# Optimization experiments

Hardware: AMD Instinct MI355X
Metric: run time of the kernel (lower is better)

Reference implementation:

```python
import jax, jax.numpy as jnp
import numpy as np
import math

B, S, HID = 128, 200, 1024
NH = 4
DK = HID // NH
LSESS = 200  # session_len
MAXSEQ = 200
EPS = 1e-12


def setup_inputs() -> dict:
    key = jax.random.key(0)
    ks = jax.random.split(key, 12)
    inp = {}
    inp['query'] = jax.random.normal(ks[0], (B, S, HID), jnp.float32)
    inp['key'] = jax.random.normal(ks[1], (B, S, HID), jnp.float32)
    inp['value'] = jax.random.normal(ks[2], (B, S, HID), jnp.float32)
    std = 0.05
    inp['attn_w0'] = std * jax.random.normal(ks[3], (DK, DK), jnp.float32)
    inp['attn_w1'] = std * jax.random.normal(ks[4], (DK, DK), jnp.float32)
    inp['attn_w2'] = std * jax.random.normal(ks[5], (DK, DK), jnp.float32)
    inp['attn_w3'] = std * jax.random.normal(ks[6], (LSESS, DK), jnp.float32)
    inp['attn_bias'] = jnp.zeros((DK,), jnp.float32)
    inp['complex_weight'] = 0.02 * jax.random.normal(ks[7], (1, NH, MAXSEQ // 2 + 1, DK, 2), jnp.float32)
    bound = 1.0 / math.sqrt(HID)
    inp['linear_w'] = jax.random.uniform(ks[8], (HID, HID), jnp.float32, -bound, bound)
    inp['linear_b'] = jax.random.uniform(ks[9], (HID,), jnp.float32, -bound, bound)
    inp['ln_w'] = jnp.ones((HID,), jnp.float32)
    inp['ln_b'] = jnp.zeros((HID,), jnp.float32)
    return inp


def _gelu(x):
    return x * 0.5 * (1.0 + jax.lax.erf(x / jnp.sqrt(jnp.asarray(2.0, x.dtype))))


def reference(query, key, value, attn_w0, attn_w1, attn_w2, attn_w3, attn_bias,
              complex_weight, linear_w, linear_b, ln_w, ln_b):
    nb = query.shape[0]
    # (B, S, H, DK) -> (B, H, S, DK)
    def split_heads(x):
        return x.reshape(nb, -1, NH, DK).transpose(0, 2, 1, 3)
    q, k, v = split_heads(query), split_heads(key), split_heads(value)

    q = q @ attn_w0
    k = k @ attn_w1
    v = v @ attn_w2

    qf = jnp.fft.rfft(q, axis=2, norm='ortho')   # (B,H,S//2+1,DK) complex
    kf = jnp.fft.rfft(k, axis=2, norm='ortho')
    weight = complex_weight[..., 0] + 1j * complex_weight[..., 1]  # (1,4,MAXSEQ//2+1,DK)
    res = qf * jnp.conj(kf) * weight
    corr = jnp.fft.irfft(res, n=MAXSEQ, axis=2, norm='ortho')       # (B,H,MAXSEQ,DK)

    alpha = jnp.matmul(jax.nn.relu(corr + attn_bias), attn_w3.T)    # (B,H,MAXSEQ,LSESS)
    alpha = jax.nn.softmax(alpha, axis=-2)                          # softmax over seq dim
    x = jnp.einsum('bhsl,bhsd->bhld', alpha, v)                     # (B,H,LSESS,DK)

    x = x.transpose(0, 2, 1, 3).reshape(nb, -1, NH * DK)            # (B,LSESS,HID)
    x = x @ linear_w.T + linear_b
    # dropout is identity at inference
    x = _gelu(x)
    # LayerNorm (TF-style, eps inside sqrt)
    u = x.mean(-1, keepdims=True)
    s = ((x - u) ** 2).mean(-1, keepdims=True)
    x = (x - u) / jnp.sqrt(s + EPS)
    return ln_w * x + ln_b
```

## Files before the change

### kernel.cpp

```cpp
#include <hip/hip_runtime.h>
#include <hip/hip_bf16.h>
#include <math.h>

#define BATCH 128
#define SEQ   200
#define HID   1024
#define NH    4
#define DK    256
#define NF    101
#define NF2   202
#define LS    200
#define PD    256

typedef __attribute__((ext_vector_type(8))) short bf16x8;
typedef __attribute__((ext_vector_type(4))) float f32x4;

__device__ __forceinline__ unsigned short f2bf(float f) {
    union { float f; unsigned u; } v; v.f = f;
    unsigned r = v.u + 0x7fff + ((v.u >> 16) & 1);
    return (unsigned short)(r >> 16);
}
__device__ __forceinline__ float bf2f(unsigned short h) {
    union { unsigned u; float f; } v; v.u = ((unsigned)h) << 16;
    return v.f;
}

__device__ __forceinline__ void gld_lds16(const void* g, void* l) {
    __builtin_amdgcn_global_load_lds(
        (const __attribute__((address_space(1))) unsigned*)g,
        (__attribute__((address_space(3))) unsigned*)l, 16, 0, 0);
}

#define KSWZ(row, c8) ((c8) ^ (((row) & 7) << 3))

__global__ void init_tables_bf16(unsigned short* __restrict__ F, unsigned short* __restrict__ G) {
    int idx = blockIdx.x * 256 + threadIdx.x;
    const double inv = 0.07071067811865475244;
    const double PI2 = 6.283185307179586476925;
    {
        int fidx = idx >> 8, s = idx & 255;
        double v = 0.0;
        if (s < SEQ && fidx < NF2) {
            int f = (fidx < NF) ? fidx : fidx - NF;
            double ang = PI2 * (double)((f * s) % SEQ) / (double)SEQ;
            v = (fidx < NF) ? cos(ang) * inv : -sin(ang) * inv;
        }
        F[idx] = f2bf((float)v);
    }
    {
        int s = idx >> 8, j = idx & 255;
        double v = 0.0;
        if (s < SEQ && j < NF2) {
            if (j < NF) {
                double al = (j == 0 || j == NF - 1) ? 1.0 : 2.0;
                v = al * cos(PI2 * (double)((j * s) % SEQ) / (double)SEQ) * inv;
            } else {
                int f = j - NF;
                if (f != 0 && f != NF - 1)
                    v = -2.0 * sin(PI2 * (double)((f * s) % SEQ) / (double)SEQ) * inv;
            }
        }
        G[idx] = f2bf((float)v);
    }
}

__global__ void wtrans256(const float* __restrict__ src, unsigned short* __restrict__ dst) {
    int dout = blockIdx.x, din = threadIdx.x;
    dst[dout * 256 + din] = f2bf(src[din * 256 + dout]);
}

__global__ void w3pad(const float* __restrict__ src, unsigned short* __restrict__ dst) {
    int row = blockIdx.x, col = threadIdx.x;
    dst[row * 256 + col] = (row < LS) ? f2bf(src[row * 256 + col]) : (unsigned short)0;
}

__global__ void fconv(const float* __restrict__ src, unsigned short* __restrict__ dst, int n) {
    int i = blockIdx.x * 256 + threadIdx.x;
    if (i < n) dst[i] = f2bf(src[i]);
}

__global__ __launch_bounds__(256)
void mgemm128(const unsigned short* __restrict__ A, const float* __restrict__ Bf0,
              unsigned short* __restrict__ C0,
              int K, int lda, int ldb, int ldc,
              long aOuter, long aInner, long bOuter, long bInner,
              long cOuter, long cInner, int nInner, int nbValid) {
    int bz = blockIdx.z;
    int bo = bz / nInner, bi = bz - bo * nInner;
    const unsigned short* Ab = A + bo * aOuter + bi * aInner;
    const float* Bf = Bf0 + bo * bOuter + bi * bInner;

    __shared__ unsigned short As[128 * 64];
    __shared__ unsigned short Bs[128 * 64];

    int t = threadIdx.x;
    int m0 = blockIdx.y * 128, n0 = blockIdx.x * 128;
    int lane = t & 63, wave = t >> 6;
    int wr = wave >> 1, wc = wave & 1;
    int la = lane & 15, hi = lane >> 4;

    f32x4 acc[4][4] = {};
    int rsub = t >> 3;
    int c8 = (t & 7) * 8;

    for (int k0 = 0; k0 < K; k0 += 64) {
#pragma unroll
        for (int p = 0; p < 4; ++p) {
            int row = p * 32 + rsub;
            gld_lds16(Ab + (long)(m0 + row) * lda + k0 + KSWZ(row, c8), &As[row * 64 + c8]);
        }
#pragma unroll
        for (int p = 0; p < 4; ++p) {
            int row = p * 32 + rsub;
            int gn = n0 + row;
            unsigned short tmp[8];
            if (gn < nbValid) {
                const float4* src = reinterpret_cast<const float4*>(Bf + (long)gn * ldb + k0 + c8);
                float4 x0 = src[0], x1 = src[1];
                tmp[0] = f2bf(x0.x); tmp[1] = f2bf(x0.y); tmp[2] = f2bf(x0.z); tmp[3] = f2bf(x0.w);
                tmp[4] = f2bf(x1.x); tmp[5] = f2bf(x1.y); tmp[6] = f2bf(x1.z); tmp[7] = f2bf(x1.w);
            } else {
#pragma unroll
                for (int j = 0; j < 8; ++j) tmp[j] = 0;
            }
            *(bf16x8*)&Bs[row * 64 + KSWZ(row, c8)] = *(bf16x8*)tmp;
        }
        __syncthreads();
#pragma unroll
        for (int half = 0; half < 2; ++half) {
            int ko = half * 32 + hi * 8;
            bf16x8 a[4], b[4];
#pragma unroll
            for (int mi = 0; mi < 4; ++mi) {
                int ra = wr * 64 + mi * 16 + la;
                a[mi] = *(const bf16x8*)&As[ra * 64 + KSWZ(ra, ko)];
            }
#pragma unroll
            for (int ni = 0; ni < 4; ++ni) {
                int rb = wc * 64 + ni * 16 + la;
                b[ni] = *(const bf16x8*)&Bs[rb * 64 + KSWZ(rb, ko)];
            }
#pragma unroll
            for (int mi = 0; mi < 4; ++mi)
#pragma unroll
                for (int ni = 0; ni < 4; ++ni)
                    acc[mi][ni] = __builtin_amdgcn_mfma_f32_16x16x32_bf16(a[mi], b[ni], acc[mi][ni], 0, 0, 0);
        }
        __syncthreads();
    }

    unsigned short* Ch = C0 + bo * cOuter + bi * cInner;
#pragma unroll
    for (int mi = 0; mi < 4; ++mi) {
#pragma unroll
        for (int ni = 0; ni < 4; ++ni) {
            int gn = n0 + wc * 64 + ni * 16 + la;
            int gmB = m0 + wr * 64 + mi * 16 + hi * 4;
#pragma unroll
            for (int rr = 0; rr < 4; ++rr)
                Ch[(long)(gmB + rr) * ldc + gn] = f2bf(acc[mi][ni][rr]);
        }
    }
}

template <int EPI, bool XCDSWZ>
__global__ __launch_bounds__(512, 2)
void mgemm256(const unsigned short* __restrict__ A, const unsigned short* __restrict__ B,
              unsigned short* __restrict__ C0, int K, int lda, int ldb, int ldc,
              long aOuter, long aInner, long bOuter, long bInner,
              long cOuter, long cInner, int nInner, int mValid,
              const float* __restrict__ biasN) {
    extern __shared__ unsigned short lds[];
    unsigned short* AsB = lds;
    unsigned short* BsB = lds + 32768;

    int bx = blockIdx.x, by = blockIdx.y;
    if (XCDSWZ) {
        int nwg = gridDim.x * gridDim.y;
        int flat = by * gridDim.x + bx;
        int cpx = nwg >> 3;
        int swz = (flat & 7) * cpx + (flat >> 3);
        bx = swz % gridDim.x; by = swz / gridDim.x;
    }
    int bz = blockIdx.z;
    int bo = bz / nInner, bi = bz - bo * nInner;
    const unsigned short* Ab = A + bo * aOuter + bi * aInner;
    const unsigned short* Bb = B + bo * bOuter + bi * bInner;

    int t = threadIdx.x;
    int m0 = by * 256, n0 = bx * 256;
    int lane = t & 63, wave = t >> 6;
    int wr = wave >> 2, wc = wave & 3;
    int la = lane & 15, hi = lane >> 4;

    f32x4 acc[8][4] = {};
    int rsub = t >> 3;
    int c8 = (t & 7) * 8;

    auto STAGE = [&](int buf, int kt) {
        int k0 = kt << 6;
        unsigned short* Asb = AsB + buf * 16384;
        unsigned short* Bsb = BsB + buf * 16384;
#pragma unroll
        for (int p = 0; p < 4; ++p) {
            int row = p * 64 + rsub;
            int ksw = k0 + KSWZ(row, c8);
            gld_lds16(Ab + (long)(m0 + row) * lda + ksw, &Asb[row * 64 + c8]);
            gld_lds16(Bb + (long)(n0 + row) * ldb + ksw, &Bsb[row * 64 + c8]);
        }
    };

    int nkt = K >> 6;
    STAGE(0, 0);

    for (int kt = 0; kt < nkt; ++kt) {
        int cur = kt & 1;
        if (kt + 1 < nkt) {
            STAGE(cur ^ 1, kt + 1);
            asm volatile("s_waitcnt vmcnt(8)" ::: "memory");
        } else {
            asm volatile("s_waitcnt vmcnt(0)" ::: "memory");
        }
        __builtin_amdgcn_s_barrier();
        const unsigned short* Acur = AsB + cur * 16384;
        const unsigned short* Bcur = BsB + cur * 16384;
#pragma unroll
        for (int half = 0; half < 2; ++half) {
            int ko = half * 32 + hi * 8;
            bf16x8 a[8], b[4];
#pragma unroll
            for (int mi = 0; mi < 8; ++mi) {
                int ra = wr * 128 + mi * 16 + la;
                a[mi] = *(const bf16x8*)&Acur[ra * 64 + KSWZ(ra, ko)];
            }
#pragma unroll
            for (int ni = 0; ni < 4; ++ni) {
                int rb = wc * 64 + ni * 16 + la;
                b[ni] = *(const bf16x8*)&Bcur[rb * 64 + KSWZ(rb, ko)];
            }
            __builtin_amdgcn_s_setprio(1);
#pragma unroll
            for (int mi = 0; mi < 8; ++mi)
#pragma unroll
                for (int ni = 0; ni < 4; ++ni)
                    acc[mi][ni] = __builtin_amdgcn_mfma_f32_16x16x32_bf16(a[mi], b[ni], acc[mi][ni], 0, 0, 0);
            __builtin_amdgcn_s_setprio(0);
        }
        __builtin_amdgcn_s_barrier();
    }

    unsigned short* Ch = C0 + bo * cOuter + bi * cInner;
#pragma unroll
    for (int mi = 0; mi < 8; ++mi) {
#pragma unroll
        for (int ni = 0; ni < 4; ++ni) {
            int gn = n0 + wc * 64 + ni * 16 + la;
            int gmB = m0 + wr * 128 + mi * 16 + hi * 4;
            float bN = 0.f;
            if (EPI == 2 || EPI == 4) bN = biasN[gn];
#pragma unroll
            for (int rr = 0; rr < 4; ++rr) {
                int gm = gmB + rr;
                if (gm >= mValid) continue;
                float v = acc[mi][ni][rr];
                if (EPI == 0) Ch[(long)gm * ldc + gn] = f2bf(v);
                else if (EPI == 2) Ch[(long)gm * ldc + gn] = f2bf(fmaxf(v + bN, 0.f));
                else Ch[(long)gm * ldc + gn] = f2bf(v + bN);
            }
        }
    }
}

__global__ void crossspec(unsigned short* __restrict__ QF, const unsigned short* __restrict__ KF,
                          const float* __restrict__ cw) {
    long idx = (long)blockIdx.x * 256 + threadIdx.x;
    if (idx >= (long)BATCH * NH * DK * NF) return;
    int f = (int)(idx % NF);
    long tq = idx / NF;
    int d = (int)(tq % DK);
    int bh = (int)(tq / DK);
    int h = bh & (NH - 1);
    long base = (long)bh * DK * PD + (long)d * PD;
    float qr = bf2f(QF[base + f]), qi = bf2f(QF[base + NF + f]);
    float kr = bf2f(KF[base + f]), ki = bf2f(KF[base + NF + f]);
    float cr = qr * kr + qi * ki;
    float ci = qi * kr - qr * ki;
    long wb = (((long)h * NF + f) * DK + d) * 2;
    float wr = cw[wb], wi = cw[wb + 1];
    QF[base + f]      = f2bf(cr * wr - ci * wi);
    QF[base + NF + f] = f2bf(cr * wi + ci * wr);
    if (f < PD - NF2) QF[base + NF2 + f] = 0;
}

__global__ __launch_bounds__(256) void softmax_rows(const unsigned short* __restrict__ in,
                                                    unsigned short* __restrict__ out) {
    long row = (long)blockIdx.x * 4 + (threadIdx.x >> 6);
    int lane = threadIdx.x & 63;
    const unsigned short* p = in + row * PD;
    float v[4];
    float m = -1e30f;
#pragma unroll
    for (int i = 0; i < 4; ++i) {
        int s = lane + 64 * i;
        v[i] = (s < SEQ) ? bf2f(p[s]) : -1e30f;
        m = fmaxf(m, v[i]);
    }
#pragma unroll
    for (int o = 32; o; o >>= 1) m = fmaxf(m, __shfl_xor(m, o));
    float e[4], sum = 0.f;
#pragma unroll
    for (int i = 0; i < 4; ++i) {
        int s = lane + 64 * i;
        e[i] = (s < SEQ) ? expf(v[i] - m) : 0.f;
        sum += e[i];
    }
#pragma unroll
    for (int o = 32; o; o >>= 1) sum += __shfl_xor(sum, o);
    float inv = 1.f / sum;
    unsigned short* q = out + row * PD;
#pragma unroll
    for (int i = 0; i < 4; ++i) {
        int s = lane + 64 * i;
        q[s] = (s < SEQ) ? f2bf(e[i] * inv) : (unsigned short)0;
    }
}

__global__ __launch_bounds__(256) void gelu_ln_kernel(const unsigned short* __restrict__ y2,
                               const float* __restrict__ lnw, const float* __restrict__ lnb,
                               float* __restrict__ out) {
    long row = blockIdx.x;
    int tid = threadIdx.x;
    const short4* xr = reinterpret_cast<const short4*>(y2 + row * HID);
    short4 h4 = xr[tid];
    float g[4];
    {
        float x0 = bf2f((unsigned short)h4.x), x1 = bf2f((unsigned short)h4.y);
        float x2 = bf2f((unsigned short)h4.z), x3 = bf2f((unsigned short)h4.w);
        g[0] = 0.5f * x0 * (1.f + erff(x0 * 0.70710678118654752f));
        g[1] = 0.5f * x1 * (1.f + erff(x1 * 0.70710678118654752f));
        g[2] = 0.5f * x2 * (1.f + erff(x2 * 0.70710678118654752f));
        g[3] = 0.5f * x3 * (1.f + erff(x3 * 0.70710678118654752f));
    }

    __shared__ float red[4];
    float s = g[0] + g[1] + g[2] + g[3];
#pragma unroll
    for (int o = 32; o > 0; o >>= 1) s += __shfl_down(s, o);
    if ((tid & 63) == 0) red[tid >> 6] = s;
    __syncthreads();
    float mean = (red[0] + red[1] + red[2] + red[3]) * (1.f / (float)HID);

    float v2 = 0.f;
#pragma unroll
    for (int p = 0; p < 4; ++p) { float d = g[p] - mean; v2 += d * d; }
    __syncthreads();
#pragma unroll
    for (int o = 32; o > 0; o >>= 1) v2 += __shfl_down(v2, o);
    if ((tid & 63) == 0) red[tid >> 6] = v2;
    __syncthreads();
    float var = (red[0] + red[1] + red[2] + red[3]) * (1.f / (float)HID);
    float rstd = rsqrtf(var + 1e-12f);

    float4 o4;
    int i0 = tid * 4;
    o4.x = (g[0] - mean) * rstd * lnw[i0 + 0] + lnb[i0 + 0];
    o4.y = (g[1] - mean) * rstd * lnw[i0 + 1] + lnb[i0 + 1];
    o4.z = (g[2] - mean) * rstd * lnw[i0 + 2] + lnb[i0 + 2];
    o4.w = (g[3] - mean) * rstd * lnw[i0 + 3] + lnb[i0 + 3];
    reinterpret_cast<float4*>(out + row * HID)[tid] = o4;
}

extern "C" void kernel_launch(void* const* d_in, const int* in_sizes, int n_in,
                              void* d_out, int out_size, void* d_ws, size_t ws_size,
                              hipStream_t stream) {
    const float* query = (const float*)d_in[0];
    const float* key   = (const float*)d_in[1];
    const float* value = (const float*)d_in[2];
    const float* w0 = (const float*)d_in[3];
    const float* w1 = (const float*)d_in[4];
    const float* w2 = (const float*)d_in[5];
    const float* w3 = (const float*)d_in[6];
    const float* attn_bias = (const float*)d_in[7];
    const float* cw = (const float*)d_in[8];
    const float* lw = (const float*)d_in[9];
    const float* lb = (const float*)d_in[10];
    const float* lnw = (const float*)d_in[11];
    const float* lnb = (const float*)d_in[12];
    float* out = (float*)d_out;

    char* base = (char*)d_ws;
    const long BH = (long)BATCH * NH;
    const long SZR = (long)BH * PD * PD;
    const size_t M64 = 67108864;

    unsigned short* F_stack = (unsigned short*)(base + 0);
    unsigned short* G_stack = (unsigned short*)(base + 131072);
    unsigned short* w0T = (unsigned short*)(base + 262144);
    unsigned short* w1T = (unsigned short*)(base + 393216);
    unsigned short* w2T = (unsigned short*)(base + 524288);
    unsigned short* w3b = (unsigned short*)(base + 655360);
    unsigned short* lwb = (unsigned short*)(base + 786432);
    char* rA = base + 4194304;
    char* rB = rA + M64;
    char* rC = rB + M64;
    char* rD = rC + M64;
    char* rE = rD + M64;

    unsigned short* qpT = (unsigned short*)rA;
    unsigned short* kpT = (unsigned short*)rB;
    unsigned short* vpT = (unsigned short*)rC;
    unsigned short* QF  = (unsigned short*)rD;
    unsigned short* KF  = (unsigned short*)rE;
    unsigned short* corr = (unsigned short*)rA;
    unsigned short* alphaT = (unsigned short*)rD;
    unsigned short* probs = (unsigned short*)rB;
    unsigned short* X  = (unsigned short*)rE;
    unsigned short* y2 = (unsigned short*)rD;

    const size_t LDS256 = 131072;

    init_tables_bf16<<<256, 256, 0, stream>>>(F_stack, G_stack);
    wtrans256<<<256, 256, 0, stream>>>(w0, w0T);
    wtrans256<<<256, 256, 0, stream>>>(w1, w1T);
    wtrans256<<<256, 256, 0, stream>>>(w2, w2T);
    w3pad<<<256, 256, 0, stream>>>(w3, w3b);
    fconv<<<(HID * HID + 255) / 256, 256, 0, stream>>>(lw, lwb, HID * HID);

    dim3 gproj(2, 2, BH);
    mgemm128<<<gproj, 256, 0, stream>>>(w0T, query, qpT, DK, DK, HID, PD,
        0L, 0L, (long)SEQ * HID, (long)DK, (long)NH * PD * PD, (long)PD * PD, NH, SEQ);
    mgemm128<<<gproj, 256, 0, stream>>>(w1T, key, kpT, DK, DK, HID, PD,
        0L, 0L, (long)SEQ * HID, (long)DK, (long)NH * PD * PD, (long)PD * PD, NH, SEQ);
    mgemm128<<<gproj, 256, 0, stream>>>(w2T, value, vpT, DK, DK, HID, PD,
        0L, 0L, (long)SEQ * HID, (long)DK, (long)NH * PD * PD, (long)PD * PD, NH, SEQ);

    mgemm256<0, false><<<dim3(1, 1, 2 * BH), 512, LDS256, stream>>>(
        qpT, F_stack, QF, PD, PD, PD, PD,
        SZR, (long)PD * PD, 0L, 0L, SZR, (long)PD * PD, (int)BH, PD, nullptr);

    long ncs = (long)BH * DK * NF;
    crossspec<<<(unsigned)((ncs + 255) / 256), 256, 0, stream>>>(QF, KF, cw);

    mgemm256<2, false><<<dim3(1, 1, BH), 512, LDS256, stream>>>(
        G_stack, QF, corr, PD, PD, PD, PD,
        0L, 0L, (long)PD * PD, 0L, (long)PD * PD, 0L, 1, PD, attn_bias);

    mgemm256<0, false><<<dim3(1, 1, BH), 512, LDS256, stream>>>(
        w3b, corr, alphaT, PD, PD, PD, PD,
        0L, 0L, (long)PD * PD, 0L, (long)PD * PD, 0L, 1, PD, nullptr);

    softmax_rows<<<(unsigned)(BH * PD / 4), 256, 0, stream>>>(alphaT, probs);

    mgemm256<0, false><<<dim3(1, 1, BH), 512, LDS256, stream>>>(
        probs, vpT, X, PD, PD, PD, HID,
        (long)NH * PD * PD, (long)PD * PD,
        (long)NH * PD * PD, (long)PD * PD,
        (long)LS * HID, (long)DK, NH, LS, nullptr);

    mgemm256<4, true><<<dim3(HID / 256, (BATCH * LS) / 256, 1), 512, LDS256, stream>>>(
        X, lwb, y2, HID, HID, HID, HID,
        0L, 0L, 0L, 0L, 0L, 0L, 1, BATCH * LS, lb);

    gelu_ln_kernel<<<(unsigned)(BATCH * LS), 256, 0, stream>>>(y2, lnw, lnb, out);
}
```

Baseline: 615.5 us.

## Interleave next-tile global-to-LDS staging with quarter-phase MFMA blocks in GEMM loop

The bf16 MFMA GEMM main loop is split into four phases per k-tile. Each phase issues a quarter of the next tile's global-to-LDS loads and then runs a batch of 16 MFMAs on half the A rows and half the K slice. This spreads memory issue across the compute and lowers the number of live A fragment registers, with the aim of hiding load latency and easing register pressure. In exchange, each k-tile now takes four workgroup barriers instead of two, and the waitcnt logic becomes finer-grained.

```diff
diff --git a/kernel.cpp b/kernel.cpp
--- a/kernel.cpp
+++ b/kernel.cpp
@@ -197,57 +197,113 @@
     int rsub = t >> 3;
     int c8 = (t & 7) * 8;
 
-    auto STAGE = [&](int buf, int kt) {
-        int k0 = kt << 6;
-        unsigned short* Asb = AsB + buf * 16384;
-        unsigned short* Bsb = BsB + buf * 16384;
-#pragma unroll
-        for (int p = 0; p < 4; ++p) {
-            int row = p * 64 + rsub;
-            int ksw = k0 + KSWZ(row, c8);
-            gld_lds16(Ab + (long)(m0 + row) * lda + ksw, &Asb[row * 64 + c8]);
-            gld_lds16(Bb + (long)(n0 + row) * ldb + ksw, &Bsb[row * 64 + c8]);
+    auto stageA = [&](unsigned short* dst, long k0, int h) {
+#pragma unroll
+        for (int p = 0; p < 2; ++p) {
+            int row = h * 128 + p * 64 + rsub;
+            gld_lds16(Ab + (long)(m0 + row) * lda + k0 + KSWZ(row, c8), &dst[row * 64 + c8]);
         }
     };
+    auto stageB = [&](unsigned short* dst, long k0, int h) {
+#pragma unroll
+        for (int p = 0; p < 2; ++p) {
+            int row = h * 128 + p * 64 + rsub;
+            gld_lds16(Bb + (long)(n0 + row) * ldb + k0 + KSWZ(row, c8), &dst[row * 64 + c8]);
+        }
+    };
+    auto ldf = [&](const unsigned short* P, int row, int ko) -> bf16x8 {
+        return *(const bf16x8*)&P[row * 64 + KSWZ(row, ko)];
+    };
+
+#define MFMA_ROW(mi, xa) \
+    acc[mi][0] = __builtin_amdgcn_mfma_f32_16x16x32_bf16(xa, b0, acc[mi][0], 0, 0, 0); \
+    acc[mi][1] = __builtin_amdgcn_mfma_f32_16x16x32_bf16(xa, b1, acc[mi][1], 0, 0, 0); \
+    acc[mi][2] = __builtin_amdgcn_mfma_f32_16x16x32_bf16(xa, b2, acc[mi][2], 0, 0, 0); \
+    acc[mi][3] = __builtin_amdgcn_mfma_f32_16x16x32_bf16(xa, b3, acc[mi][3], 0, 0, 0);
 
     int nkt = K >> 6;
-    STAGE(0, 0);
+    stageA(AsB, 0, 0); stageA(AsB, 0, 1);
+    stageB(BsB, 0, 0); stageB(BsB, 0, 1);
 
     for (int kt = 0; kt < nkt; ++kt) {
         int cur = kt & 1;
-        if (kt + 1 < nkt) {
-            STAGE(cur ^ 1, kt + 1);
-            asm volatile("s_waitcnt vmcnt(8)" ::: "memory");
+        const unsigned short* Ac = AsB + cur * 16384;
+        const unsigned short* Bc = BsB + cur * 16384;
+        unsigned short* An = AsB + (cur ^ 1) * 16384;
+        unsigned short* Bn = BsB + (cur ^ 1) * 16384;
+        bool pre = (kt + 1) < nkt;
+        long kn = (long)(kt + 1) << 6;
+
+        bf16x8 b0, b1, b2, b3;
+
+        if (pre) {
+            stageA(An, kn, 0);
+            asm volatile("s_waitcnt vmcnt(2)" ::: "memory");
         } else {
             asm volatile("s_waitcnt vmcnt(0)" ::: "memory");
         }
         __builtin_amdgcn_s_barrier();
-        const unsigned short* Acur = AsB + cur * 16384;
-        const unsigned short* Bcur = BsB + cur * 16384;
-#pragma unroll
-        for (int half = 0; half < 2; ++half) {
-            int ko = half * 32 + hi * 8;
-            bf16x8 a[8], b[4];
-#pragma unroll
-            for (int mi = 0; mi < 8; ++mi) {
-                int ra = wr * 128 + mi * 16 + la;
-                a[mi] = *(const bf16x8*)&Acur[ra * 64 + KSWZ(ra, ko)];
-            }
-#pragma unroll
-            for (int ni = 0; ni < 4; ++ni) {
-                int rb = wc * 64 + ni * 16 + la;
-                b[ni] = *(const bf16x8*)&Bcur[rb * 64 + KSWZ(rb, ko)];
-            }
+        __builtin_amdgcn_sched_barrier(0);
+        {
+            int ko = hi * 8;
+            b0 = ldf(Bc, wc * 64 + 0 * 16 + la, ko);
+            b1 = ldf(Bc, wc * 64 + 1 * 16 + la, ko);
+            b2 = ldf(Bc, wc * 64 + 2 * 16 + la, ko);
+            b3 = ldf(Bc, wc * 64 + 3 * 16 + la, ko);
+            bf16x8 x0 = ldf(Ac, wr * 128 + 0 * 16 + la, ko);
+            bf16x8 x1 = ldf(Ac, wr * 128 + 1 * 16 + la, ko);
+            bf16x8 x2 = ldf(Ac, wr * 128 + 2 * 16 + la, ko);
+            bf16x8 x3 = ldf(Ac, wr * 128 + 3 * 16 + la, ko);
             __builtin_amdgcn_s_setprio(1);
-#pragma unroll
-            for (int mi = 0; mi < 8; ++mi)
-#pragma unroll
-                for (int ni = 0; ni < 4; ++ni)
-                    acc[mi][ni] = __builtin_amdgcn_mfma_f32_16x16x32_bf16(a[mi], b[ni], acc[mi][ni], 0, 0, 0);
+            MFMA_ROW(0, x0) MFMA_ROW(1, x1) MFMA_ROW(2, x2) MFMA_ROW(3, x3)
             __builtin_amdgcn_s_setprio(0);
         }
         __builtin_amdgcn_s_barrier();
-    }
+
+        if (pre) stageA(An, kn, 1);
+        {
+            int ko = hi * 8;
+            bf16x8 x4 = ldf(Ac, wr * 128 + 4 * 16 + la, ko);
+            bf16x8 x5 = ldf(Ac, wr * 128 + 5 * 16 + la, ko);
+            bf16x8 x6 = ldf(Ac, wr * 128 + 6 * 16 + la, ko);
+            bf16x8 x7 = ldf(Ac, wr * 128 + 7 * 16 + la, ko);
+            __builtin_amdgcn_s_setprio(1);
+            MFMA_ROW(4, x4) MFMA_ROW(5, x5) MFMA_ROW(6, x6) MFMA_ROW(7, x7)
+            __builtin_amdgcn_s_setprio(0);
+        }
+        __builtin_amdgcn_s_barrier();
+
+        if (pre) stageB(Bn, kn, 0);
+        {
+            int ko = 32 + hi * 8;
+            b0 = ldf(Bc, wc * 64 + 0 * 16 + la, ko);
+            b1 = ldf(Bc, wc * 64 + 1 * 16 + la, ko);
+            b2 = ldf(Bc, wc * 64 + 2 * 16 + la, ko);
+            b3 = ldf(Bc, wc * 64 + 3 * 16 + la, ko);
+            bf16x8 x0 = ldf(Ac, wr * 128 + 0 * 16 + la, ko);
+            bf16x8 x1 = ldf(Ac, wr * 128 + 1 * 16 + la, ko);
+            bf16x8 x2 = ldf(Ac, wr * 128 + 2 * 16 + la, ko);
+            bf16x8 x3 = ldf(Ac, wr * 128 + 3 * 16 + la, ko);
+            __builtin_amdgcn_s_setprio(1);
+            MFMA_ROW(0, x0) MFMA_ROW(1, x1) MFMA_ROW(2, x2) MFMA_ROW(3, x3)
+            __builtin_amdgcn_s_setprio(0);
+        }
+        __builtin_amdgcn_s_barrier();
+
+        if (pre) stageB(Bn, kn, 1);
+        {
+            int ko = 32 + hi * 8;
+            bf16x8 x4 = ldf(Ac, wr * 128 + 4 * 16 + la, ko);
+            bf16x8 x5 = ldf(Ac, wr * 128 + 5 * 16 + la, ko);
+            bf16x8 x6 = ldf(Ac, wr * 128 + 6 * 16 + la, ko);
+            bf16x8 x7 = ldf(Ac, wr * 128 + 7 * 16 + la, ko);
+            __builtin_amdgcn_s_setprio(1);
+            MFMA_ROW(4, x4) MFMA_ROW(5, x5) MFMA_ROW(6, x6) MFMA_ROW(7, x7)
+            __builtin_amdgcn_s_setprio(0);
+        }
+        __builtin_amdgcn_s_barrier();
+    }
+#undef MFMA_ROW
 
     unsigned short* Ch = C0 + bo * cOuter + bi * cInner;
 #pragma unroll
```

After: 605.1 us. No clear change (-1.7%).
